# Kernel tuning notes

Measured on AMD Instinct MI355X. Metric: run time of the kernel, lower is better.

Reference implementation:

```python
import jax, jax.numpy as jnp
import numpy as np

DROPOUT_P = 0.1  # module-level constant in the source
DROP_KEY = jax.random.key(42)

B, H, S, D = 4, 16, 1024, 64


def setup_inputs() -> dict:
    key = jax.random.key(0)
    kq, kk, kv = jax.random.split(key, 3)
    return {
        "query": jax.random.normal(kq, (B, H, S, D), dtype=jnp.float32),
        "key": jax.random.normal(kk, (B, H, S, D), dtype=jnp.float32),
        "value": jax.random.normal(kv, (B, H, S, D), dtype=jnp.float32),
        "scale_factor": 8,
    }


def reference(query, key, value, scale_factor):
    # qk = query @ key^T                         [B,H,S,S]
    qk = jnp.einsum("bhqd,bhkd->bhqk", query, key)
    # source divides by inv_scale = 1/scale_factor -> multiply by scale_factor
    scaled_qk = qk * jnp.float32(scale_factor)
    softmax_qk = jax.nn.softmax(scaled_qk, axis=-1)
    # inverted dropout with fixed key (deterministic reference)
    keep = jax.random.bernoulli(DROP_KEY, 1.0 - DROPOUT_P, softmax_qk.shape)
    dropout_qk = jnp.where(keep, softmax_qk / (1.0 - DROPOUT_P), 0.0)
    # output = attn @ value                      [B,H,S,D]
    return jnp.einsum("bhqk,bhkd->bhqd", dropout_qk, value)
```

## Files before the change

kernel.cpp:

```cpp
#include <hip/hip_runtime.h>
#include <hip/hip_bf16.h>
#include <stdint.h>
#include <math.h>


constexpr int Bn = 4, Hn = 16, Sn = 1024, Dn = 64;
constexpr int NT = 256;
constexpr int TK = 64;
constexpr int TQM = 64;
constexpr int CAP = 128;

typedef short s16x8 __attribute__((ext_vector_type(8)));
typedef short s16x4 __attribute__((ext_vector_type(4)));
typedef float f32x4 __attribute__((ext_vector_type(4)));

__device__ __forceinline__ uint16_t f2bf(float x) {
  uint32_t u = __float_as_uint(x);
  return (uint16_t)((u + 0x7fffu + ((u >> 16) & 1u)) >> 16);
}
__device__ __forceinline__ uint16_t f2bf_fast(float x) {
  return __builtin_bit_cast(uint16_t, __float2bfloat16(x));
}
__device__ __forceinline__ float bf2f(uint16_t h) {
  return __uint_as_float(((uint32_t)h) << 16);
}
__device__ __forceinline__ float fexp2(float x) {
  return __builtin_amdgcn_exp2f(x);
}

__device__ __forceinline__ void tf_round(uint32_t& x0, uint32_t& x1, const int r) {
  x0 += x1;
  x1 = (x1 << r) | (x1 >> (32 - r));
  x1 ^= x0;
}

__device__ __noinline__ int keep_bit(uint32_t j) {
  uint32_t x0 = 0u, x1 = j;
  const uint32_t k0 = 0u, k1v = 42u;
  const uint32_t k2v = k0 ^ k1v ^ 0x1BD11BDAu;
  x0 += k0; x1 += k1v;
  tf_round(x0, x1, 13); tf_round(x0, x1, 15); tf_round(x0, x1, 26); tf_round(x0, x1, 6);
  x0 += k1v; x1 += k2v + 1u;
  tf_round(x0, x1, 17); tf_round(x0, x1, 29); tf_round(x0, x1, 16); tf_round(x0, x1, 24);
  x0 += k2v; x1 += k0 + 2u;
  tf_round(x0, x1, 13); tf_round(x0, x1, 15); tf_round(x0, x1, 26); tf_round(x0, x1, 6);
  x0 += k0; x1 += k1v + 3u;
  tf_round(x0, x1, 17); tf_round(x0, x1, 29); tf_round(x0, x1, 16); tf_round(x0, x1, 24);
  x0 += k1v; x1 += k2v + 4u;
  tf_round(x0, x1, 13); tf_round(x0, x1, 15); tf_round(x0, x1, 26); tf_round(x0, x1, 6);
  x0 += k2v; x1 += k0 + 5u;
  uint32_t bits = x0 ^ x1;
  float u = __uint_as_float((bits >> 9) | 0x3f800000u) - 1.0f;
  return u < 0.9f;
}

__global__ __launch_bounds__(NT) void prep_kv(const float* __restrict__ K,
                                              const float* __restrict__ V,
                                              uint16_t* __restrict__ Khg,
                                              uint16_t* __restrict__ Klg,
                                              uint16_t* __restrict__ Vtg) {
  __shared__ float Vl[TK][Dn + 1];
  const int t = threadIdx.x;
  const int kt = blockIdx.x;
  const int bh = blockIdx.y;
  const int r = t >> 2, qd = t & 3;
  const size_t tile = ((size_t)bh * 16 + kt) * 4096;
  const float* ksrc = K + ((size_t)bh * Sn + (size_t)(kt * TK + r)) * Dn + qd * 16;
  const float* vsrc = V + ((size_t)bh * Sn + (size_t)(kt * TK + r)) * Dn + qd * 16;

#pragma unroll
  for (int half = 0; half < 2; ++half) {
    float4 a = *(const float4*)(ksrc + half * 8);
    float4 b = *(const float4*)(ksrc + half * 8 + 4);
    float xs[8] = {a.x, a.y, a.z, a.w, b.x, b.y, b.z, b.w};
    s16x8 hv, lv;
#pragma unroll
    for (int j = 0; j < 8; ++j) {
      uint16_t hb = f2bf(xs[j]);
      hv[j] = (short)hb;
      lv[j] = (short)f2bf(xs[j] - bf2f(hb));
    }
    const int sc = (qd * 2 + half) ^ (r & 7);
    *(s16x8*)&Khg[tile + (size_t)r * 64 + sc * 8] = hv;
    *(s16x8*)&Klg[tile + (size_t)r * 64 + sc * 8] = lv;
    float4 va = *(const float4*)(vsrc + half * 8);
    float4 vb = *(const float4*)(vsrc + half * 8 + 4);
    *(float4*)&Vl[r][qd * 16 + half * 8] = va;
    *(float4*)&Vl[r][qd * 16 + half * 8 + 4] = vb;
  }
  __syncthreads();
#pragma unroll
  for (int half = 0; half < 2; ++half) {
    s16x8 ov;
#pragma unroll
    for (int j = 0; j < 8; ++j) ov[j] = (short)f2bf(Vl[qd * 16 + half * 8 + j][r]);
    const int sc = (qd * 2 + half) ^ (r & 7);
    *(s16x8*)&Vtg[tile + (size_t)r * 64 + sc * 8] = ov;
  }
}

__global__ __launch_bounds__(NT, 4) void attn_mfma7(
    const float* __restrict__ Q, const uint16_t* __restrict__ Khg,
    const uint16_t* __restrict__ Klg, const uint16_t* __restrict__ Vtg,
    const float* __restrict__ V, const int* __restrict__ scale_ptr,
    float* __restrict__ out) {
  __shared__ uint16_t KhS[TK * Dn];
  __shared__ uint16_t KlS[TK * Dn];
  __shared__ uint16_t VtS[TK * Dn];
  __shared__ uint16_t PS[4 * 16 * 64];
  __shared__ uint32_t Lm[4][CAP];
  __shared__ float Lsv[4][CAP];
  __shared__ float mfin[4][16];

  const int t = threadIdx.x;
  const int w = t >> 6;
  const int lane = t & 63;
  const int l16 = lane & 15;
  const int quad = lane >> 4;
  const int xl = l16 & 7;

  const int b = blockIdx.z, h = blockIdx.y;
  const int qbase = blockIdx.x * TQM;
  const int bh = b * Hn + h;
  const float qscale = (float)(*scale_ptr) * 1.44269504089f;
  const float pthr = 1.670170079e-5f;

  const int e0off = (w * 2) * 512 + lane * 8;
  const int e1off = (w * 2 + 1) * 512 + lane * 8;
  const size_t tbase = (size_t)bh * 16 * 4096;
  const int psw = w * 1024;

  s16x8 qh[2], ql[2];
  {
    const int qrow = qbase + w * 16 + l16;
    const float* src = Q + ((size_t)bh * Sn + (size_t)qrow) * Dn;
#pragma unroll
    for (int ks = 0; ks < 2; ++ks) {
      float4 x0 = *(const float4*)(src + ks * 32 + quad * 8);
      float4 x1 = *(const float4*)(src + ks * 32 + quad * 8 + 4);
      float xv[8] = {x0.x, x0.y, x0.z, x0.w, x1.x, x1.y, x1.z, x1.w};
#pragma unroll
      for (int j = 0; j < 8; ++j) {
        const float xs = xv[j] * qscale;
        uint16_t hb = f2bf_fast(xs);
        qh[ks][j] = (short)hb;
        ql[ks][j] = (short)f2bf_fast(xs - bf2f(hb));
      }
    }
  }

  float m_r = -INFINITY, l_r = 0.0f;
  f32x4 o_acc[4];
#pragma unroll
  for (int c = 0; c < 4; ++c) o_acc[c] = (f32x4){0.f, 0.f, 0.f, 0.f};

  const uint32_t hbase = (uint32_t)bh * (uint32_t)Sn;
  int lbase = 0;

  for (int kt = 0; kt < Sn / TK; ++kt) {
    const int kbase = kt * TK;
    __syncthreads();

    {
      const size_t tile = tbase + (size_t)kt * 4096;
      __builtin_amdgcn_global_load_lds(
          (const __attribute__((address_space(1))) uint32_t*)(Khg + tile + e0off),
          (__attribute__((address_space(3))) uint32_t*)(KhS + e0off), 16, 0, 0);
      __builtin_amdgcn_global_load_lds(
          (const __attribute__((address_space(1))) uint32_t*)(Khg + tile + e1off),
          (__attribute__((address_space(3))) uint32_t*)(KhS + e1off), 16, 0, 0);
      __builtin_amdgcn_global_load_lds(
          (const __attribute__((address_space(1))) uint32_t*)(Klg + tile + e0off),
          (__attribute__((address_space(3))) uint32_t*)(KlS + e0off), 16, 0, 0);
      __builtin_amdgcn_global_load_lds(
          (const __attribute__((address_space(1))) uint32_t*)(Klg + tile + e1off),
          (__attribute__((address_space(3))) uint32_t*)(KlS + e1off), 16, 0, 0);
      __builtin_amdgcn_global_load_lds(
          (const __attribute__((address_space(1))) uint32_t*)(Vtg + tile + e0off),
          (__attribute__((address_space(3))) uint32_t*)(VtS + e0off), 16, 0, 0);
      __builtin_amdgcn_global_load_lds(
          (const __attribute__((address_space(1))) uint32_t*)(Vtg + tile + e1off),
          (__attribute__((address_space(3))) uint32_t*)(VtS + e1off), 16, 0, 0);
    }
    __syncthreads();

    f32x4 sacc[4];
#pragma unroll
    for (int c = 0; c < 4; ++c) sacc[c] = (f32x4){0.f, 0.f, 0.f, 0.f};
#pragma unroll
    for (int ks = 0; ks < 2; ++ks) {
#pragma unroll
      for (int c = 0; c < 4; ++c) {
        const int boff = (c * 16 + l16) * 64 + (((ks * 4 + quad) ^ xl) * 8);
        const s16x8 khv = *(const s16x8*)&KhS[boff];
        const s16x8 klv = *(const s16x8*)&KlS[boff];
        sacc[c] = __builtin_amdgcn_mfma_f32_16x16x32_bf16(khv, qh[ks], sacc[c], 0, 0, 0);
        sacc[c] = __builtin_amdgcn_mfma_f32_16x16x32_bf16(khv, ql[ks], sacc[c], 0, 0, 0);
        sacc[c] = __builtin_amdgcn_mfma_f32_16x16x32_bf16(klv, qh[ks], sacc[c], 0, 0, 0);
      }
    }

    {
      float mx = sacc[0][0];
#pragma unroll
      for (int c = 0; c < 4; ++c)
#pragma unroll
        for (int r = 0; r < 4; ++r) mx = fmaxf(mx, sacc[c][r]);
      mx = fmaxf(mx, __shfl_xor(mx, 16));
      mx = fmaxf(mx, __shfl_xor(mx, 32));

      if (__ballot(mx > m_r) != 0ull) {
        const float mn = fmaxf(m_r, mx);
        const float al = fexp2(m_r - mn);
        m_r = mn;
#pragma unroll
        for (int c = 0; c < 4; ++c)
#pragma unroll
          for (int r = 0; r < 4; ++r) o_acc[c][r] *= al;
        l_r *= al;
      }

      const bool anyhot = __ballot(mx - m_r > -15.88f) != 0ull;
      float rs = 0.0f;
#pragma unroll
      for (int c = 0; c < 4; ++c) {
        float pc[4];
#pragma unroll
        for (int r = 0; r < 4; ++r) {
          pc[r] = fexp2(sacc[c][r] - m_r);
          rs += pc[r];
        }
        if (anyhot) {
#pragma unroll
          for (int r = 0; r < 4; ++r) {
            const uint64_t mc = __ballot(pc[r] > pthr);
            if (mc != 0ull) {
              if (lbase + 64 <= CAP) {
                const int slot = lbase + (int)__popcll(mc & ((1ull << lane) - 1ull));
                if (pc[r] > pthr) {
                  Lm[w][slot] = ((uint32_t)l16 << 10) |
                                (uint32_t)(kbase + c * 16 + quad * 4 + r);
                  Lsv[w][slot] = sacc[c][r];
                }
                lbase += (int)__popcll(mc);
              } else if (pc[r] > pthr) {
                const uint32_t j =
                    (hbase + (uint32_t)(qbase + w * 16 + l16)) * (uint32_t)Sn +
                    (uint32_t)(kbase + c * 16 + quad * 4 + r);
                if (!keep_bit(j)) pc[r] = 0.0f;
              }
            }
          }
        }
        s16x4 pk;
#pragma unroll
        for (int r = 0; r < 4; ++r) pk[r] = (short)f2bf_fast(pc[r]);
        const int pos = (c * 2 + (quad >> 1)) ^ xl;
        *(s16x4*)&PS[psw + l16 * 64 + pos * 8 + (quad & 1) * 4] = pk;
      }

      rs += __shfl_xor(rs, 16);
      rs += __shfl_xor(rs, 32);
      l_r += rs;
    }

#pragma unroll
    for (int ks2 = 0; ks2 < 2; ++ks2) {
      const s16x8 pb = *(const s16x8*)&PS[psw + l16 * 64 + (((ks2 * 4 + quad) ^ xl) * 8)];
#pragma unroll
      for (int c = 0; c < 4; ++c) {
        const int voff = (c * 16 + l16) * 64 + (((ks2 * 4 + quad) ^ xl) * 8);
        const s16x8 vb = *(const s16x8*)&VtS[voff];
        o_acc[c] = __builtin_amdgcn_mfma_f32_16x16x32_bf16(vb, pb, o_acc[c], 0, 0, 0);
      }
    }
  }

  if (quad == 0) mfin[w][l16] = m_r;
  for (int e0 = 0; e0 < lbase; e0 += 64) {
    const int e = e0 + lane;
    const bool valid = e < lbase;
    const uint32_t meta = valid ? Lm[w][e] : 0u;
    const float sv = valid ? Lsv[w][e] : 0.0f;
    const uint32_t rwv = meta >> 10, keyv = meta & 1023u;
    const uint32_t grow = (uint32_t)(qbase + w * 16) + rwv;
    const uint32_t j = (hbase + grow) * (uint32_t)Sn + keyv;
    const int kb = keep_bit(j);
    uint64_t dm = __ballot(valid && !kb);
    while (dm != 0ull) {
      const int src = (int)__builtin_ctzll(dm);
      dm &= dm - 1ull;
      const uint32_t meta_s = (uint32_t)__builtin_amdgcn_readlane((int)meta, src);
      const float sv_s =
          __uint_as_float((uint32_t)__builtin_amdgcn_readlane((int)__float_as_uint(sv), src));
      const int rw = (int)(meta_s >> 10);
      const int key = (int)(meta_s & 1023u);
      const float p = fexp2(sv_s - mfin[w][rw]);
      const float pb2 = bf2f(f2bf_fast(p));
      if (rw == l16) {
        const float* vp = V + ((size_t)bh * Sn + (size_t)key) * Dn;
#pragma unroll
        for (int c = 0; c < 4; ++c) {
          float4 vv = *(const float4*)(vp + c * 16 + quad * 4);
          o_acc[c][0] = fmaf(-pb2, bf2f(f2bf(vv.x)), o_acc[c][0]);
          o_acc[c][1] = fmaf(-pb2, bf2f(f2bf(vv.y)), o_acc[c][1]);
          o_acc[c][2] = fmaf(-pb2, bf2f(f2bf(vv.z)), o_acc[c][2]);
          o_acc[c][3] = fmaf(-pb2, bf2f(f2bf(vv.w)), o_acc[c][3]);
        }
      }
    }
  }

  {
    const float inv = 1.0f / (l_r * 0.9f);
    const size_t obase = ((size_t)bh * Sn + (size_t)(qbase + w * 16 + l16)) * Dn;
#pragma unroll
    for (int c = 0; c < 4; ++c) {
      float4 ov;
      ov.x = o_acc[c][0] * inv;
      ov.y = o_acc[c][1] * inv;
      ov.z = o_acc[c][2] * inv;
      ov.w = o_acc[c][3] * inv;
      *(float4*)(out + obase + c * 16 + quad * 4) = ov;
    }
  }
}

constexpr int KST = 72;
__global__ __launch_bounds__(NT) void attn_fallback(
    const float* __restrict__ Q, const float* __restrict__ K,
    const float* __restrict__ V, const int* __restrict__ scale_ptr,
    float* __restrict__ out) {
  __shared__ uint16_t KhS[64 * KST];
  __shared__ uint16_t KlS[64 * KST];
  __shared__ uint16_t VtS[Dn * KST];
  __shared__ uint16_t PSf[4 * 16 * KST];

  const int t = threadIdx.x;
  const int w = t >> 6;
  const int lane = t & 63;
  const int l16 = lane & 15;
  const int quad = lane >> 4;
  const int b = blockIdx.z, h = blockIdx.y;
  const int qbase = blockIdx.x * 64;
  const size_t bh = (size_t)b * Hn + h;
  const float scale = (float)(*scale_ptr);
  const float* Kp = K + bh * Sn * Dn;
  const float* Vp = V + bh * Sn * Dn;

  const int qrow = qbase + w * 16 + l16;
  const float* Qp = Q + (bh * Sn + (size_t)qrow) * Dn;
  s16x8 qh[2], ql[2];
#pragma unroll
  for (int ks = 0; ks < 2; ++ks) {
    const float* src = Qp + ks * 32 + quad * 8;
    float4 x0 = *(const float4*)(src);
    float4 x1 = *(const float4*)(src + 4);
    float xv[8] = {x0.x, x0.y, x0.z, x0.w, x1.x, x1.y, x1.z, x1.w};
#pragma unroll
    for (int j = 0; j < 8; ++j) {
      uint16_t hb = f2bf(xv[j]);
      qh[ks][j] = (short)hb;
      ql[ks][j] = (short)f2bf(xv[j] - bf2f(hb));
    }
  }
  const int kr = t >> 2;
  const int qd = t & 3;
  float m_r[4], l_r[4];
#pragma unroll
  for (int r = 0; r < 4; ++r) { m_r[r] = -INFINITY; l_r[r] = 0.0f; }
  f32x4 o_acc[4];
#pragma unroll
  for (int c = 0; c < 4; ++c) o_acc[c] = (f32x4){0.f, 0.f, 0.f, 0.f};
  const uint32_t rowlin = ((uint32_t)(b * Hn + h)) * (uint32_t)Sn +
                          (uint32_t)(qbase + w * 16 + quad * 4);
  for (int kt = 0; kt < Sn / 64; ++kt) {
    const int kbase = kt * 64;
    __syncthreads();
    {
      const float* ksrc = Kp + (size_t)(kbase + kr) * Dn + qd * 16;
#pragma unroll
      for (int half = 0; half < 2; ++half) {
        float4 a = *(const float4*)(ksrc + half * 8);
        float4 b2 = *(const float4*)(ksrc + half * 8 + 4);
        float xs[8] = {a.x, a.y, a.z, a.w, b2.x, b2.y, b2.z, b2.w};
        s16x8 hv, lv;
#pragma unroll
        for (int j = 0; j < 8; ++j) {
          uint16_t hb = f2bf(xs[j]);
          hv[j] = (short)hb;
          lv[j] = (short)f2bf(xs[j] - bf2f(hb));
        }
        *(s16x8*)&KhS[kr * KST + qd * 16 + half * 8] = hv;
        *(s16x8*)&KlS[kr * KST + qd * 16 + half * 8] = lv;
      }
      const float* vsrc = Vp + (size_t)(kbase + kr) * Dn + qd * 16;
#pragma unroll
      for (int half = 0; half < 2; ++half) {
        float4 a = *(const float4*)(vsrc + half * 8);
        float4 b2 = *(const float4*)(vsrc + half * 8 + 4);
        float xs[8] = {a.x, a.y, a.z, a.w, b2.x, b2.y, b2.z, b2.w};
#pragma unroll
        for (int j = 0; j < 8; ++j)
          VtS[(qd * 16 + half * 8 + j) * KST + kr] = f2bf(xs[j]);
      }
    }
    __syncthreads();
    f32x4 sacc[4];
#pragma unroll
    for (int c = 0; c < 4; ++c) sacc[c] = (f32x4){0.f, 0.f, 0.f, 0.f};
#pragma unroll
    for (int ks = 0; ks < 2; ++ks) {
#pragma unroll
      for (int c = 0; c < 4; ++c) {
        const s16x8 bh_ = *(const s16x8*)&KhS[(c * 16 + l16) * KST + ks * 32 + quad * 8];
        const s16x8 bl_ = *(const s16x8*)&KlS[(c * 16 + l16) * KST + ks * 32 + quad * 8];
        sacc[c] = __builtin_amdgcn_mfma_f32_16x16x32_bf16(qh[ks], bh_, sacc[c], 0, 0, 0);
        sacc[c] = __builtin_amdgcn_mfma_f32_16x16x32_bf16(ql[ks], bh_, sacc[c], 0, 0, 0);
        sacc[c] = __builtin_amdgcn_mfma_f32_16x16x32_bf16(qh[ks], bl_, sacc[c], 0, 0, 0);
      }
    }
    float mx[4];
#pragma unroll
    for (int r = 0; r < 4; ++r) {
      mx[r] = sacc[0][r] * scale;
#pragma unroll
      for (int c = 1; c < 4; ++c) mx[r] = fmaxf(mx[r], sacc[c][r] * scale);
#pragma unroll
      for (int d = 1; d < 16; d <<= 1) mx[r] = fmaxf(mx[r], __shfl_xor(mx[r], d));
    }
    float al[4];
#pragma unroll
    for (int r = 0; r < 4; ++r) {
      const float mn = fmaxf(m_r[r], mx[r]);
      al[r] = __expf(m_r[r] - mn);
      m_r[r] = mn;
    }
#pragma unroll
    for (int c = 0; c < 4; ++c)
#pragma unroll
      for (int r = 0; r < 4; ++r) o_acc[c][r] *= al[r];
    float rs[4] = {0.f, 0.f, 0.f, 0.f};
#pragma unroll
    for (int c = 0; c < 4; ++c) {
#pragma unroll
      for (int r = 0; r < 4; ++r) {
        const float d = sacc[c][r] * scale - m_r[r];
        float pv = __expf(d);
        rs[r] += pv;
        if (d > -25.0f) {
          const uint32_t j = (rowlin + (uint32_t)r) * (uint32_t)Sn +
                             (uint32_t)(kbase + c * 16 + l16);
          if (!keep_bit(j)) pv = 0.0f;
        }
        PSf[(w * 16 + quad * 4 + r) * KST + c * 16 + l16] = f2bf(pv);
      }
    }
#pragma unroll
    for (int r = 0; r < 4; ++r) {
#pragma unroll
      for (int d = 1; d < 16; d <<= 1) rs[r] += __shfl_xor(rs[r], d);
      l_r[r] = l_r[r] * al[r] + rs[r];
    }
#pragma unroll
    for (int ks2 = 0; ks2 < 2; ++ks2) {
      const s16x8 pa = *(const s16x8*)&PSf[(w * 16 + l16) * KST + ks2 * 32 + quad * 8];
#pragma unroll
      for (int c = 0; c < 4; ++c) {
        const s16x8 vb = *(const s16x8*)&VtS[(c * 16 + l16) * KST + ks2 * 32 + quad * 8];
        o_acc[c] = __builtin_amdgcn_mfma_f32_16x16x32_bf16(pa, vb, o_acc[c], 0, 0, 0);
      }
    }
  }
  float inv[4];
#pragma unroll
  for (int r = 0; r < 4; ++r) inv[r] = 1.0f / (l_r[r] * 0.9f);
#pragma unroll
  for (int c = 0; c < 4; ++c)
#pragma unroll
    for (int r = 0; r < 4; ++r)
      out[(bh * Sn + (size_t)(qbase + w * 16 + quad * 4 + r)) * Dn + c * 16 + l16] =
          o_acc[c][r] * inv[r];
}

extern "C" void kernel_launch(void* const* d_in, const int* in_sizes, int n_in,
                              void* d_out, int out_size, void* d_ws, size_t ws_size,
                              hipStream_t stream) {
  const float* Q = (const float*)d_in[0];
  const float* K = (const float*)d_in[1];
  const float* V = (const float*)d_in[2];
  const int* sf = (const int*)d_in[3];
  float* out = (float*)d_out;

  constexpr size_t ARR = (size_t)Bn * Hn * Sn * Dn;
  const size_t need = 3 * ARR * sizeof(uint16_t);

  if (ws_size >= need) {
    uint16_t* Khg = (uint16_t*)d_ws;
    uint16_t* Klg = Khg + ARR;
    uint16_t* Vtg = Klg + ARR;
    prep_kv<<<dim3(16, 64), NT, 0, stream>>>(K, V, Khg, Klg, Vtg);
    attn_mfma7<<<dim3(Sn / TQM, Hn, Bn), NT, 0, stream>>>(Q, Khg, Klg, Vtg, V, sf, out);
  } else {
    attn_fallback<<<dim3(Sn / 64, Hn, Bn), NT, 0, stream>>>(Q, K, V, sf, out);
  }
}
```

Before: 167.9 us.

## Double-buffer K/V tiles and widen attention blocks to eight waves

The attention kernel now uses 512 threads (8 waves, 128 query rows per block) and double-buffers the K-high, K-low and V^T tiles in LDS. The next tile's global-to-LDS loads are issued before computing on the current tile, so load latency can overlap MFMA work. Each K/V tile is also shared by twice as many query rows, which halves the tile loads per query. In exchange LDS use roughly doubles and the grid has half as many blocks (512), which may lower occupancy and leave CUs underused. The prep and fallback kernels keep 256 threads.

```diff
diff --git a/kernel.cpp b/kernel.cpp
--- a/kernel.cpp
+++ b/kernel.cpp
@@ -5,10 +5,12 @@
 
 
 constexpr int Bn = 4, Hn = 16, Sn = 1024, Dn = 64;
-constexpr int NT = 256;
+constexpr int NT = 512;
+constexpr int NTF = 256;
 constexpr int TK = 64;
-constexpr int TQM = 64;
+constexpr int TQM = 128;
 constexpr int CAP = 128;
+constexpr int NTILE = Sn / TK;
 
 typedef short s16x8 __attribute__((ext_vector_type(8)));
 typedef short s16x4 __attribute__((ext_vector_type(4)));
@@ -54,11 +56,11 @@
   return u < 0.9f;
 }
 
-__global__ __launch_bounds__(NT) void prep_kv(const float* __restrict__ K,
-                                              const float* __restrict__ V,
-                                              uint16_t* __restrict__ Khg,
-                                              uint16_t* __restrict__ Klg,
-                                              uint16_t* __restrict__ Vtg) {
+__global__ __launch_bounds__(NTF) void prep_kv(const float* __restrict__ K,
+                                               const float* __restrict__ V,
+                                               uint16_t* __restrict__ Khg,
+                                               uint16_t* __restrict__ Klg,
+                                               uint16_t* __restrict__ Vtg) {
   __shared__ float Vl[TK][Dn + 1];
   const int t = threadIdx.x;
   const int kt = blockIdx.x;
@@ -104,13 +106,13 @@
     const uint16_t* __restrict__ Klg, const uint16_t* __restrict__ Vtg,
     const float* __restrict__ V, const int* __restrict__ scale_ptr,
     float* __restrict__ out) {
-  __shared__ uint16_t KhS[TK * Dn];
-  __shared__ uint16_t KlS[TK * Dn];
-  __shared__ uint16_t VtS[TK * Dn];
-  __shared__ uint16_t PS[4 * 16 * 64];
-  __shared__ uint32_t Lm[4][CAP];
-  __shared__ float Lsv[4][CAP];
-  __shared__ float mfin[4][16];
+  __shared__ uint16_t KhS[2][TK * Dn];
+  __shared__ uint16_t KlS[2][TK * Dn];
+  __shared__ uint16_t VtS[2][TK * Dn];
+  __shared__ uint16_t PS[8 * 16 * 64];
+  __shared__ uint32_t Lm[8][CAP];
+  __shared__ float Lsv[8][CAP];
+  __shared__ float mfin[8][16];
 
   const int t = threadIdx.x;
   const int w = t >> 6;
@@ -125,10 +127,24 @@
   const float qscale = (float)(*scale_ptr) * 1.44269504089f;
   const float pthr = 1.670170079e-5f;
 
-  const int e0off = (w * 2) * 512 + lane * 8;
-  const int e1off = (w * 2 + 1) * 512 + lane * 8;
+  const int eoff = w * 512 + lane * 8;
   const size_t tbase = (size_t)bh * 16 * 4096;
   const int psw = w * 1024;
+
+  auto issue3 = [&](int ti, int pb) {
+    const size_t tile = tbase + (size_t)ti * 4096;
+    __builtin_amdgcn_global_load_lds(
+        (const __attribute__((address_space(1))) uint32_t*)(Khg + tile + eoff),
+        (__attribute__((address_space(3))) uint32_t*)(&KhS[pb][eoff]), 16, 0, 0);
+    __builtin_amdgcn_global_load_lds(
+        (const __attribute__((address_space(1))) uint32_t*)(Klg + tile + eoff),
+        (__attribute__((address_space(3))) uint32_t*)(&KlS[pb][eoff]), 16, 0, 0);
+    __builtin_amdgcn_global_load_lds(
+        (const __attribute__((address_space(1))) uint32_t*)(Vtg + tile + eoff),
+        (__attribute__((address_space(3))) uint32_t*)(&VtS[pb][eoff]), 16, 0, 0);
+  };
+
+  issue3(0, 0);
 
   s16x8 qh[2], ql[2];
   {
@@ -157,33 +173,7 @@
   const uint32_t hbase = (uint32_t)bh * (uint32_t)Sn;
   int lbase = 0;
 
-  for (int kt = 0; kt < Sn / TK; ++kt) {
-    const int kbase = kt * TK;
-    __syncthreads();
-
-    {
-      const size_t tile = tbase + (size_t)kt * 4096;
-      __builtin_amdgcn_global_load_lds(
-          (const __attribute__((address_space(1))) uint32_t*)(Khg + tile + e0off),
-          (__attribute__((address_space(3))) uint32_t*)(KhS + e0off), 16, 0, 0);
-      __builtin_amdgcn_global_load_lds(
-          (const __attribute__((address_space(1))) uint32_t*)(Khg + tile + e1off),
-          (__attribute__((address_space(3))) uint32_t*)(KhS + e1off), 16, 0, 0);
-      __builtin_amdgcn_global_load_lds(
-          (const __attribute__((address_space(1))) uint32_t*)(Klg + tile + e0off),
-          (__attribute__((address_space(3))) uint32_t*)(KlS + e0off), 16, 0, 0);
-      __builtin_amdgcn_global_load_lds(
-          (const __attribute__((address_space(1))) uint32_t*)(Klg + tile + e1off),
-          (__attribute__((address_space(3))) uint32_t*)(KlS + e1off), 16, 0, 0);
-      __builtin_amdgcn_global_load_lds(
-          (const __attribute__((address_space(1))) uint32_t*)(Vtg + tile + e0off),
-          (__attribute__((address_space(3))) uint32_t*)(VtS + e0off), 16, 0, 0);
-      __builtin_amdgcn_global_load_lds(
-          (const __attribute__((address_space(1))) uint32_t*)(Vtg + tile + e1off),
-          (__attribute__((address_space(3))) uint32_t*)(VtS + e1off), 16, 0, 0);
-    }
-    __syncthreads();
-
+  auto tile_step = [&](int kbase, int pb) {
     f32x4 sacc[4];
 #pragma unroll
     for (int c = 0; c < 4; ++c) sacc[c] = (f32x4){0.f, 0.f, 0.f, 0.f};
@@ -192,8 +182,8 @@
 #pragma unroll
       for (int c = 0; c < 4; ++c) {
         const int boff = (c * 16 + l16) * 64 + (((ks * 4 + quad) ^ xl) * 8);
-        const s16x8 khv = *(const s16x8*)&KhS[boff];
-        const s16x8 klv = *(const s16x8*)&KlS[boff];
+        const s16x8 khv = *(const s16x8*)&KhS[pb][boff];
+        const s16x8 klv = *(const s16x8*)&KlS[pb][boff];
         sacc[c] = __builtin_amdgcn_mfma_f32_16x16x32_bf16(khv, qh[ks], sacc[c], 0, 0, 0);
         sacc[c] = __builtin_amdgcn_mfma_f32_16x16x32_bf16(khv, ql[ks], sacc[c], 0, 0, 0);
         sacc[c] = __builtin_amdgcn_mfma_f32_16x16x32_bf16(klv, qh[ks], sacc[c], 0, 0, 0);
@@ -266,14 +256,23 @@
 
 #pragma unroll
     for (int ks2 = 0; ks2 < 2; ++ks2) {
-      const s16x8 pb = *(const s16x8*)&PS[psw + l16 * 64 + (((ks2 * 4 + quad) ^ xl) * 8)];
+      const s16x8 pfr = *(const s16x8*)&PS[psw + l16 * 64 + (((ks2 * 4 + quad) ^ xl) * 8)];
 #pragma unroll
       for (int c = 0; c < 4; ++c) {
         const int voff = (c * 16 + l16) * 64 + (((ks2 * 4 + quad) ^ xl) * 8);
-        const s16x8 vb = *(const s16x8*)&VtS[voff];
-        o_acc[c] = __builtin_amdgcn_mfma_f32_16x16x32_bf16(vb, pb, o_acc[c], 0, 0, 0);
-      }
-    }
+        const s16x8 vb = *(const s16x8*)&VtS[pb][voff];
+        o_acc[c] = __builtin_amdgcn_mfma_f32_16x16x32_bf16(vb, pfr, o_acc[c], 0, 0, 0);
+      }
+    }
+  };
+
+  for (int kt = 0; kt < NTILE; kt += 2) {
+    __syncthreads();
+    issue3(kt + 1, 1);
+    tile_step(kt * TK, 0);
+    __syncthreads();
+    if (kt + 2 < NTILE) issue3(kt + 2, 0);
+    tile_step((kt + 1) * TK, 1);
   }
 
   if (quad == 0) mfin[w][l16] = m_r;
@@ -327,7 +326,7 @@
 }
 
 constexpr int KST = 72;
-__global__ __launch_bounds__(NT) void attn_fallback(
+__global__ __launch_bounds__(NTF) void attn_fallback(
     const float* __restrict__ Q, const float* __restrict__ K,
     const float* __restrict__ V, const int* __restrict__ scale_ptr,
     float* __restrict__ out) {
@@ -499,9 +498,9 @@
     uint16_t* Khg = (uint16_t*)d_ws;
     uint16_t* Klg = Khg + ARR;
     uint16_t* Vtg = Klg + ARR;
-    prep_kv<<<dim3(16, 64), NT, 0, stream>>>(K, V, Khg, Klg, Vtg);
+    prep_kv<<<dim3(16, 64), NTF, 0, stream>>>(K, V, Khg, Klg, Vtg);
     attn_mfma7<<<dim3(Sn / TQM, Hn, Bn), NT, 0, stream>>>(Q, Khg, Klg, Vtg, V, sf, out);
   } else {
-    attn_fallback<<<dim3(Sn / 64, Hn, Bn), NT, 0, stream>>>(Q, K, V, sf, out);
-  }
-}
+    attn_fallback<<<dim3(Sn / 64, Hn, Bn), NTF, 0, stream>>>(Q, K, V, sf, out);
+  }
+}
```

Result: faster. 162.3 us (-3.3%).
